# Optimization experiments

Hardware: AMD Instinct MI355X
Metric: run time of the kernel (lower is better)

Reference implementation:

```python
import jax, jax.numpy as jnp
import numpy as np

D_MODEL = 1024
H = 16
D_K = D_MODEL // H
D_FF = 4096
EPS = 1e-5
NEG = -1e9


def setup_inputs() -> dict:
    key = jax.random.key(0)
    ks = jax.random.split(key, 12)
    B, S = 4, 1024
    s = 1.0 / np.sqrt(D_MODEL)
    inp = {
        'x': jax.random.normal(ks[0], (B, S, D_MODEL), dtype=jnp.float32),
        'src_mask': jax.random.randint(ks[1], (B, 1, 1, S), 0, 2, dtype=jnp.int32),
        'wq': jax.random.normal(ks[2], (D_MODEL, D_MODEL), dtype=jnp.float32) * s,
        'bq': jnp.zeros((D_MODEL,), jnp.float32),
        'wk': jax.random.normal(ks[3], (D_MODEL, D_MODEL), dtype=jnp.float32) * s,
        'bk': jnp.zeros((D_MODEL,), jnp.float32),
        'wv': jax.random.normal(ks[4], (D_MODEL, D_MODEL), dtype=jnp.float32) * s,
        'bv': jnp.zeros((D_MODEL,), jnp.float32),
        'wo': jax.random.normal(ks[5], (D_MODEL, D_MODEL), dtype=jnp.float32) * s,
        'bo': jnp.zeros((D_MODEL,), jnp.float32),
        'w1': jax.random.normal(ks[6], (D_MODEL, D_FF), dtype=jnp.float32) * s,
        'b1': jnp.zeros((D_FF,), jnp.float32),
        'w2': jax.random.normal(ks[7], (D_FF, D_MODEL), dtype=jnp.float32) * (1.0 / np.sqrt(D_FF)),
        'b2': jnp.zeros((D_MODEL,), jnp.float32),
        'ln1_a': jnp.ones((1,), jnp.float32),
        'ln1_b': jnp.zeros((1,), jnp.float32),
        'ln2_a': jnp.ones((1,), jnp.float32),
        'ln2_b': jnp.zeros((1,), jnp.float32),
    }
    return inp


def _layernorm(x, alpha, bias):
    # Matches torch: mean over last dim; std is UNBIASED (ddof=1); divide by (std + eps).
    mean = jnp.mean(x, axis=-1, keepdims=True)
    std = jnp.sqrt(jnp.var(x, axis=-1, keepdims=True, ddof=1))
    return alpha * (x - mean) / (std + EPS) + bias


def _attention(xn, src_mask, wq, bq, wk, bk, wv, bv, wo, bo):
    B, S, _ = xn.shape
    q = (xn @ wq + bq).reshape(B, S, H, D_K).transpose(0, 2, 1, 3)  # [B,H,S,Dk]
    k = (xn @ wk + bk).reshape(B, S, H, D_K).transpose(0, 2, 1, 3)
    v = (xn @ wv + bv).reshape(B, S, H, D_K).transpose(0, 2, 1, 3)
    scores = jnp.einsum('bhqd,bhkd->bhqk', q, k) / np.sqrt(D_K)
    scores = jnp.where(src_mask == 0, NEG, scores)
    # NOTE: original module applies NO softmax (faithful to source).
    out = jnp.einsum('bhqk,bhkd->bhqd', scores, v)  # [B,H,S,Dk]
    out = out.transpose(0, 2, 1, 3).reshape(B, S, D_MODEL)
    return out @ wo + bo


def reference(x, src_mask, wq, bq, wk, bk, wv, bv, wo, bo,
              w1, b1, w2, b2, ln1_a, ln1_b, ln2_a, ln2_b):
    # Pre-norm residual 1: self-attention
    x = x + _attention(_layernorm(x, ln1_a, ln1_b), src_mask,
                       wq, bq, wk, bk, wv, bv, wo, bo)
    # Pre-norm residual 2: FFN
    xn = _layernorm(x, ln2_a, ln2_b)
    ffn = jax.nn.relu(xn @ w1 + b1) @ w2 + b2
    return x + ffn
```

## Files before the change

### kernel.cpp

```cpp
#include <hip/hip_runtime.h>
#include <hip/hip_bf16.h>
#include <math.h>


#define EPS 1e-5f

typedef __attribute__((ext_vector_type(8))) short bf16x8;
typedef __attribute__((ext_vector_type(4))) float f32x4;
typedef __attribute__((ext_vector_type(8))) int i32x8;
typedef __attribute__((ext_vector_type(4))) int i32x4;

typedef const __attribute__((address_space(1))) unsigned char glob_byte;
typedef __attribute__((address_space(3))) unsigned char lds_byte;

__device__ __forceinline__ void g2l16(const void* g, void* l) {
  __builtin_amdgcn_global_load_lds((glob_byte*)g, (lds_byte*)l, 16, 0, 0);
}

__device__ __forceinline__ unsigned short f2bf(float f) {
  union { float f; unsigned int u; } v; v.f = f;
  return (unsigned short)((v.u + 0x7FFFu + ((v.u >> 16) & 1u)) >> 16);
}
__device__ __forceinline__ float bf2f(unsigned short b) {
  union { unsigned int u; float f; } v; v.u = (unsigned int)b << 16;
  return v.f;
}
__device__ __forceinline__ unsigned int fbits(float f) {
  union { float f; unsigned int u; } v; v.f = f;
  return v.u;
}
__device__ __forceinline__ unsigned int pk_fp8x4(float a, float b, float c, float d) {
  unsigned int p = 0;
  p = __builtin_amdgcn_cvt_pk_fp8_f32(a, b, p, false);
  p = __builtin_amdgcn_cvt_pk_fp8_f32(c, d, p, true);
  return p;
}

__global__ __launch_bounds__(256) void wconv_ln_kernel(
    const float* __restrict__ wq, const float* __restrict__ wk,
    const float* __restrict__ wv, const float* __restrict__ wo,
    const float* __restrict__ w1, const float* __restrict__ w2,
    const float* __restrict__ bq, const float* __restrict__ bk,
    const float* __restrict__ bv,
    unsigned short* __restrict__ wqkvT, unsigned short* __restrict__ woT,
    unsigned char* __restrict__ w1F8, unsigned char* __restrict__ w2F8,
    float* __restrict__ bqkv,
    const float* __restrict__ x, unsigned short* __restrict__ xn,
    const float* __restrict__ ln1a, const float* __restrict__ ln1b) {
  __shared__ float tile[64][65];
  const int bid = blockIdx.x;
  const int t = threadIdx.x;
  if (bid >= 3073) {
    const int row = bid - 3073;
    const float4 v = ((const float4*)(x + (size_t)row * 1024))[t];
    float s  = v.x + v.y + v.z + v.w;
    float ss = v.x * v.x + v.y * v.y + v.z * v.z + v.w * v.w;
#pragma unroll
    for (int off = 32; off > 0; off >>= 1) {
      s  += __shfl_down(s, off, 64);
      ss += __shfl_down(ss, off, 64);
    }
    __shared__ float red[8];
    const int lane = t & 63, wv_ = t >> 6;
    if (lane == 0) { red[wv_] = s; red[4 + wv_] = ss; }
    __syncthreads();
    const float S  = red[0] + red[1] + red[2] + red[3];
    const float SS = red[4] + red[5] + red[6] + red[7];
    const float mean = S * (1.0f / 1024.0f);
    float var = (SS - 1024.0f * mean * mean) * (1.0f / 1023.0f);
    var = fmaxf(var, 0.0f);
    const float scl = ln1a[0] / (sqrtf(var) + EPS);
    const float b = ln1b[0];
    ushort4 o;
    o.x = f2bf((v.x - mean) * scl + b);
    o.y = f2bf((v.y - mean) * scl + b);
    o.z = f2bf((v.z - mean) * scl + b);
    o.w = f2bf((v.w - mean) * scl + b);
    ((ushort4*)(xn + (size_t)row * 1024))[t] = o;
    return;
  }
  if (bid == 3072) {
#pragma unroll
    for (int i = 0; i < 12; ++i) {
      const int n = i * 256 + t;
      bqkv[n] = n < 1024 ? bq[n] : (n < 2048 ? bk[n - 1024] : bv[n - 2048]);
    }
    return;
  }
  const float* src; int K, N, tk, tn;
  unsigned short* dst16 = nullptr; unsigned char* dst8 = nullptr;
  if (bid < 1024) {
    const int m = bid >> 8, loc = bid & 255;
    src = m == 0 ? wq : m == 1 ? wk : m == 2 ? wv : wo;
    dst16 = m == 3 ? woT : (wqkvT + (size_t)m * 1024 * 1024);
    K = 1024; N = 1024; tk = loc >> 4; tn = loc & 15;
  } else if (bid < 2048) {
    const int loc = bid - 1024; src = w1; dst8 = w1F8;
    K = 1024; N = 4096; tk = loc >> 6; tn = loc & 63;
  } else {
    const int loc = bid - 2048; src = w2; dst8 = w2F8;
    K = 4096; N = 1024; tk = loc >> 4; tn = loc & 15;
  }
  const int lr = t >> 4, lc = (t & 15) * 4;
#pragma unroll
  for (int i = 0; i < 4; ++i) {
    const float4 v = *(const float4*)(src + (size_t)(tk * 64 + lr + 16 * i) * N + tn * 64 + lc);
    tile[lr + 16 * i][lc + 0] = v.x;
    tile[lr + 16 * i][lc + 1] = v.y;
    tile[lr + 16 * i][lc + 2] = v.z;
    tile[lr + 16 * i][lc + 3] = v.w;
  }
  __syncthreads();
  const int on = t >> 2, ok = (t & 3) * 16;
#pragma unroll
  for (int jj = 0; jj < 4; ++jj) {
    if (dst8) {
      const unsigned int p = pk_fp8x4(tile[ok + 4 * jj + 0][on], tile[ok + 4 * jj + 1][on],
                                      tile[ok + 4 * jj + 2][on], tile[ok + 4 * jj + 3][on]);
      *(unsigned int*)(dst8 + (size_t)(tn * 64 + on) * K + tk * 64 + ok + 4 * jj) = p;
    } else {
      ushort4 o4;
      o4.x = f2bf(tile[ok + 4 * jj + 0][on]);
      o4.y = f2bf(tile[ok + 4 * jj + 1][on]);
      o4.z = f2bf(tile[ok + 4 * jj + 2][on]);
      o4.w = f2bf(tile[ok + 4 * jj + 3][on]);
      *(ushort4*)(dst16 + (size_t)(tn * 64 + on) * K + tk * 64 + ok + 4 * jj) = o4;
    }
  }
}

template <int TM, int TN, bool OUT_BF16, bool RELU, bool RES, bool VSPLIT,
          int RX, int RY>
__global__ __launch_bounds__(256, 4) void mfma_gemm(
    const unsigned short* __restrict__ A, const unsigned short* __restrict__ Bt,
    const float* __restrict__ bias, const float* __restrict__ res,
    void* __restrict__ C0, void* __restrict__ C1,
    int N, int lda, int ldb, int KH) {
  constexpr int WM = 2, WN = 2;
  constexpr int MSPAN = TM / WM, NSPAN = TN / WN;
  constexpr int MI = MSPAN / 16, NJ = NSPAN / 16;
  __shared__ __align__(16) unsigned short As[TM * 64];
  __shared__ __align__(16) unsigned short Bs[TN * 64];
  const int tid = threadIdx.x, lane = tid & 63;
  const int w = tid >> 6;
  const int quad = lane >> 4, col = lane & 15;
  const int wm = w % WM, wn = w / WM;

  int bx = blockIdx.x, by = blockIdx.y;
  {
    const int gx = gridDim.x;
    const int L = bx + gx * by;
    const int r = L & 7, s = L >> 3;
    const int nrx = gx / RX;
    const int rx = r % nrx, ry = r / nrx;
    bx = rx * RX + s % RX;
    by = ry * RY + (s / RX) % RY;
  }
  const int m0 = by * TM, n0 = bx * TN;

  f32x4 acc[MI][NJ];
  const f32x4 z4 = {0.f, 0.f, 0.f, 0.f};
#pragma unroll
  for (int i = 0; i < MI; ++i)
#pragma unroll
    for (int j = 0; j < NJ; ++j) acc[i][j] = z4;

  for (int k0 = 0; k0 < KH; k0 += 64) {
    __syncthreads();
#pragma unroll
    for (int t = 0; t < TM / 32; ++t) {
      const int s = t * 256 + tid;
      const int r = s >> 3, c = (s & 7) ^ (r & 7);
      g2l16(A + (size_t)(m0 + r) * lda + k0 + c * 8, (void*)(As + s * 8));
    }
#pragma unroll
    for (int t = 0; t < TN / 32; ++t) {
      const int s = t * 256 + tid;
      const int r = s >> 3, c = (s & 7) ^ (r & 7);
      g2l16(Bt + (size_t)(n0 + r) * ldb + k0 + c * 8, (void*)(Bs + s * 8));
    }
    __syncthreads();
#pragma unroll
    for (int h = 0; h < 2; ++h) {
      bf16x8 af[MI], bfr[NJ];
#pragma unroll
      for (int i = 0; i < MI; ++i) {
        const int rr = wm * MSPAN + i * 16 + col;
        af[i] = *(const bf16x8*)(As + rr * 64 + (((h << 2) | quad) ^ (rr & 7)) * 8);
      }
#pragma unroll
      for (int j = 0; j < NJ; ++j) {
        const int rr = wn * NSPAN + j * 16 + col;
        bfr[j] = *(const bf16x8*)(Bs + rr * 64 + (((h << 2) | quad) ^ (rr & 7)) * 8);
      }
#pragma unroll
      for (int i = 0; i < MI; ++i)
#pragma unroll
        for (int j = 0; j < NJ; ++j)
          acc[i][j] = __builtin_amdgcn_mfma_f32_16x16x32_bf16(af[i], bfr[j], acc[i][j], 0, 0, 0);
    }
  }
#pragma unroll
  for (int i = 0; i < MI; ++i) {
    const int mrow = m0 + wm * MSPAN + i * 16 + quad * 4;
#pragma unroll
    for (int j = 0; j < NJ; ++j) {
      const int n = n0 + wn * NSPAN + j * 16 + col;
      const float bn = bias[n];
      if (VSPLIT && n0 >= 2048) {
        ushort4 o4;
        o4.x = f2bf(acc[i][j][0] + bn);
        o4.y = f2bf(acc[i][j][1] + bn);
        o4.z = f2bf(acc[i][j][2] + bn);
        o4.w = f2bf(acc[i][j][3] + bn);
        *(ushort4*)((unsigned short*)C1 + (size_t)(n - 2048) * 4096 + mrow) = o4;
        continue;
      }
#pragma unroll
      for (int r = 0; r < 4; ++r) {
        const int m = mrow + r;
        float v = acc[i][j][r] + bn;
        if (RES)  v += res[(size_t)m * N + n];
        if (RELU) v = fmaxf(v, 0.f);
        if (OUT_BF16) ((unsigned short*)C0)[(size_t)m * N + n] = f2bf(v);
        else          ((float*)C0)[(size_t)m * N + n] = v;
      }
    }
  }
}

template <bool FP8OUT, int TN, int RX, int RY>
__global__ __launch_bounds__(256, 4) void mfma_gemm_fp8(
    const unsigned char* __restrict__ A, const unsigned char* __restrict__ Bt,
    const float* __restrict__ bias, const unsigned short* __restrict__ res16,
    void* __restrict__ C0, int N, int lda, int ldb, int KH) {
  constexpr int NSPAN = TN / 2;
  constexpr int NJ = NSPAN / 16;
  __shared__ __align__(16) unsigned char As[128 * 128];
  __shared__ __align__(16) unsigned char Bs[TN * 128];
  const int tid = threadIdx.x, lane = tid & 63;
  const int w = tid >> 6;
  const int quad = lane >> 4, col = lane & 15;
  const int wm = w & 1, wn = w >> 1;

  int bx = blockIdx.x, by = blockIdx.y;
  {
    const int gx = gridDim.x;
    const int L = bx + gx * by;
    const int r = L & 7, s = L >> 3;
    const int nrx = gx / RX;
    const int rx = r % nrx, ry = r / nrx;
    bx = rx * RX + s % RX;
    by = ry * RY + (s / RX) % RY;
  }
  const int m0 = by * 128, n0 = bx * TN;

  f32x4 acc[4][NJ];
  const f32x4 z4 = {0.f, 0.f, 0.f, 0.f};
#pragma unroll
  for (int i = 0; i < 4; ++i)
#pragma unroll
    for (int j = 0; j < NJ; ++j) acc[i][j] = z4;

  for (int k0 = 0; k0 < KH; k0 += 128) {
    __syncthreads();
#pragma unroll
    for (int t = 0; t < 4; ++t) {
      const int s = t * 256 + tid;
      const int r = s >> 3, c = (s & 7) ^ (r & 7);
      g2l16(A + (size_t)(m0 + r) * lda + k0 + c * 16, (void*)(As + s * 16));
    }
#pragma unroll
    for (int t = 0; t < TN / 32; ++t) {
      const int s = t * 256 + tid;
      const int r = s >> 3, c = (s & 7) ^ (r & 7);
      g2l16(Bt + (size_t)(n0 + r) * ldb + k0 + c * 16, (void*)(Bs + s * 16));
    }
    __syncthreads();
    i32x8 af[4];
#pragma unroll
    for (int i = 0; i < 4; ++i) {
      const int rr = wm * 64 + i * 16 + col;
      const i32x4* rowp = (const i32x4*)(As + rr * 128);
      const i32x4 lo = rowp[(2 * quad) ^ (rr & 7)];
      const i32x4 hi = rowp[(2 * quad + 1) ^ (rr & 7)];
      af[i] = __builtin_shufflevector(lo, hi, 0, 1, 2, 3, 4, 5, 6, 7);
    }
#pragma unroll
    for (int j = 0; j < NJ; ++j) {
      const int rr = wn * NSPAN + j * 16 + col;
      const i32x4* rowp = (const i32x4*)(Bs + rr * 128);
      const i32x4 lo = rowp[(2 * quad) ^ (rr & 7)];
      const i32x4 hi = rowp[(2 * quad + 1) ^ (rr & 7)];
      const i32x8 bfj = __builtin_shufflevector(lo, hi, 0, 1, 2, 3, 4, 5, 6, 7);
#pragma unroll
      for (int i = 0; i < 4; ++i)
        acc[i][j] = __builtin_amdgcn_mfma_scale_f32_16x16x128_f8f6f4(
            af[i], bfj, acc[i][j], 0, 0, 0, 0x7F7F7F7Fu, 0, 0x7F7F7F7Fu);
    }
  }
#pragma unroll
  for (int i = 0; i < 4; ++i) {
    const int mrow = m0 + wm * 64 + i * 16 + quad * 4;
#pragma unroll
    for (int j = 0; j < NJ; ++j) {
      const int n = n0 + wn * NSPAN + j * 16 + col;
      const float bn = bias[n];
#pragma unroll
      for (int r = 0; r < 4; ++r) {
        const int m = mrow + r;
        if (FP8OUT) {
          const float v = fmaxf(acc[i][j][r] + bn, 0.f);
          const unsigned int p = __builtin_amdgcn_cvt_pk_fp8_f32(v, v, 0, false);
          ((unsigned char*)C0)[(size_t)m * N + n] = (unsigned char)(p & 0xFF);
        } else {
          const float v = acc[i][j][r] + bn + bf2f(res16[(size_t)m * N + n]);
          ((float*)C0)[(size_t)m * N + n] = v;
        }
      }
    }
  }
}

__global__ __launch_bounds__(256) void ln2_kernel(
    const unsigned short* __restrict__ x1,
    const float* __restrict__ alpha, const float* __restrict__ beta,
    unsigned char* __restrict__ xn2f8) {
  const int row = blockIdx.x, t = threadIdx.x;
  const size_t i = (size_t)row * 256 + t;
  const ushort4 a4 = ((const ushort4*)x1)[i];
  float4 v;
  v.x = bf2f(a4.x); v.y = bf2f(a4.y); v.z = bf2f(a4.z); v.w = bf2f(a4.w);
  float s  = v.x + v.y + v.z + v.w;
  float ss = v.x * v.x + v.y * v.y + v.z * v.z + v.w * v.w;
#pragma unroll
  for (int off = 32; off > 0; off >>= 1) {
    s  += __shfl_down(s, off, 64);
    ss += __shfl_down(ss, off, 64);
  }
  __shared__ float red[8];
  const int lane = t & 63, wv_ = t >> 6;
  if (lane == 0) { red[wv_] = s; red[4 + wv_] = ss; }
  __syncthreads();
  const float S  = red[0] + red[1] + red[2] + red[3];
  const float SS = red[4] + red[5] + red[6] + red[7];
  const float mean = S * (1.0f / 1024.0f);
  float var = (SS - 1024.0f * mean * mean) * (1.0f / 1023.0f);
  var = fmaxf(var, 0.0f);
  const float scl = alpha[0] / (sqrtf(var) + EPS);
  const float bb = beta[0];
  ((unsigned int*)xn2f8)[i] = pk_fp8x4((v.x - mean) * scl + bb,
                                       (v.y - mean) * scl + bb,
                                       (v.z - mean) * scl + bb,
                                       (v.w - mean) * scl + bb);
}

__global__ __launch_bounds__(256) void attn_combine_kernel(
    const unsigned short* __restrict__ p0, const unsigned short* __restrict__ p1,
    const float* __restrict__ corr, unsigned short* __restrict__ ctx) {
  const int row = blockIdx.x, t = threadIdx.x;
  const size_t i = (size_t)row * 256 + t;
  const ushort4 a4 = ((const ushort4*)p0)[i];
  const ushort4 b4 = ((const ushort4*)p1)[i];
  const float4 c4 = ((const float4*)(corr + (row >> 10) * 1024))[t];
  ushort4 o;
  o.x = f2bf(bf2f(a4.x) + bf2f(b4.x) - 1e9f * c4.x);
  o.y = f2bf(bf2f(a4.y) + bf2f(b4.y) - 1e9f * c4.y);
  o.z = f2bf(bf2f(a4.z) + bf2f(b4.z) - 1e9f * c4.z);
  o.w = f2bf(bf2f(a4.w) + bf2f(b4.w) - 1e9f * c4.w);
  ((ushort4*)ctx)[i] = o;
}

__global__ __launch_bounds__(256, 4) void attn_masksum_kernel(
    const unsigned short* __restrict__ qkb, const unsigned short* __restrict__ vT,
    const int* __restrict__ mask,
    unsigned short* __restrict__ ctxp0, unsigned short* __restrict__ ctxp1,
    float* __restrict__ corr) {
  __shared__ __align__(16) unsigned short Qs[128 * 64];
  __shared__ __align__(16) unsigned short Ks[32 * 64];
  __shared__ __align__(16) unsigned short Vs[64 * 32];
  __shared__ __align__(16) unsigned short Ps[128 * 40];
  __shared__ float redm[4][4];
  const int tid = threadIdx.x, lane = tid & 63, w = tid >> 6;

  if (blockIdx.z >= 8) {
    const int hd = blockIdx.x + 8 * (blockIdx.y + 16 * (blockIdx.z - 8));
    const int t = tid;
    float sb[4];
#pragma unroll
    for (int b = 0; b < 4; ++b) {
      const ushort4 v4 = *(const ushort4*)(vT + (size_t)hd * 4096 + b * 1024 + t * 4);
      const int4 m4 = *(const int4*)(mask + b * 1024 + t * 4);
      float s = 0.f;
      if (m4.x == 0) s += bf2f(v4.x);
      if (m4.y == 0) s += bf2f(v4.y);
      if (m4.z == 0) s += bf2f(v4.z);
      if (m4.w == 0) s += bf2f(v4.w);
#pragma unroll
      for (int off = 32; off > 0; off >>= 1) s += __shfl_down(s, off, 64);
      sb[b] = s;
    }
    if (lane == 0) {
      redm[w][0] = sb[0]; redm[w][1] = sb[1]; redm[w][2] = sb[2]; redm[w][3] = sb[3];
    }
    __syncthreads();
    if (t < 4)
      corr[t * 1024 + hd] = redm[0][t] + redm[1][t] + redm[2][t] + redm[3][t];
    return;
  }

  const int quad = lane >> 4, col = lane & 15;
  const int L = blockIdx.x + 8 * (blockIdx.y + 16 * blockIdx.z);
  const int s_ = L >> 3;
  const int g = (L & 7) * 16 + (s_ >> 3);
  const int q0 = (s_ & 7) * 128;
  const int h = g & 15, bkz = g >> 4;
  const int b = bkz >> 1, kz = bkz & 1;
  const size_t qbase = ((size_t)(b * 1024 + q0)) * 2048 + h * 64;

#pragma unroll
  for (int t = 0; t < 4; ++t) {
    const int s = t * 256 + w * 64 + lane;
    const int m = s >> 3, c = (s & 7) ^ (m & 7);
    g2l16(qkb + qbase + (size_t)m * 2048 + c * 8, (void*)(Qs + s * 8));
  }
  __syncthreads();
  bf16x8 qf[2][2];
#pragma unroll
  for (int qt = 0; qt < 2; ++qt)
#pragma unroll
    for (int kf = 0; kf < 2; ++kf) {
      const int m = (w * 2 + qt) * 16 + col;
      const int c = (kf * 4 + quad) ^ (m & 7);
      qf[qt][kf] = *(const bf16x8*)(Qs + m * 64 + c * 8);
    }

  const f32x4 z4 = {0.f, 0.f, 0.f, 0.f};
  f32x4 oacc[2][4];
#pragma unroll
  for (int qt = 0; qt < 2; ++qt)
#pragma unroll
    for (int nt = 0; nt < 4; ++nt) oacc[qt][nt] = z4;

  const int* mrow = mask + b * 1024;
  const int kb0 = kz * 512;
  for (int kb = kb0; kb < kb0 + 512; kb += 32) {
    __syncthreads();
    {
      const int s = w * 64 + lane;
      const int key = s >> 3, ck = (s & 7) ^ (key & 7);
      g2l16(qkb + ((size_t)(b * 1024 + kb + key)) * 2048 + 1024 + h * 64 + ck * 8,
            (void*)(Ks + s * 8));
      const int d = s >> 2, cv = (s & 3) ^ (((d >> 2) ^ d) & 3);
      g2l16(vT + ((size_t)(h * 64 + d)) * 4096 + b * 1024 + kb + cv * 8,
            (void*)(Vs + s * 8));
    }
    __syncthreads();

    f32x4 st[2][2];
#pragma unroll
    for (int qt = 0; qt < 2; ++qt)
#pragma unroll
      for (int kt = 0; kt < 2; ++kt) st[qt][kt] = z4;
#pragma unroll
    for (int kt = 0; kt < 2; ++kt)
#pragma unroll
      for (int kf = 0; kf < 2; ++kf) {
        const int key = kt * 16 + col;
        const int c = (kf * 4 + quad) ^ (key & 7);
        const bf16x8 kfrag = *(const bf16x8*)(Ks + key * 64 + c * 8);
#pragma unroll
        for (int qt = 0; qt < 2; ++qt)
          st[qt][kt] = __builtin_amdgcn_mfma_f32_16x16x32_bf16(
              kfrag, qf[qt][kf], st[qt][kt], 0, 0, 0);
      }

    const int4 mv0 = *(const int4*)(mrow + kb + quad * 4);
    const int4 mv1 = *(const int4*)(mrow + kb + 16 + quad * 4);
#pragma unroll
    for (int qt = 0; qt < 2; ++qt) {
      const int qrow = (w * 2 + qt) * 16 + col;
#pragma unroll
      for (int kt = 0; kt < 2; ++kt) {
        const int4 mv = kt ? mv1 : mv0;
        const f32x4 sv = st[qt][kt];
        const unsigned int u0 = fbits((mv.x ? 0.125f : 0.f) * sv[0]) + 0x8000u;
        const unsigned int u1 = fbits((mv.y ? 0.125f : 0.f) * sv[1]) + 0x8000u;
        const unsigned int u2 = fbits((mv.z ? 0.125f : 0.f) * sv[2]) + 0x8000u;
        const unsigned int u3 = fbits((mv.w ? 0.125f : 0.f) * sv[3]) + 0x8000u;
        uint2 pk;
        pk.x = (u0 >> 16) | (u1 & 0xFFFF0000u);
        pk.y = (u2 >> 16) | (u3 & 0xFFFF0000u);
        const int pp = kt * 2 + (quad >> 1);
        *(uint2*)(Ps + qrow * 40 + ((pp ^ (qrow & 3)) * 8 + (quad & 1) * 4)) = pk;
      }
    }

#pragma unroll
    for (int qt = 0; qt < 2; ++qt) {
      const int qrow = (w * 2 + qt) * 16 + col;
      const bf16x8 pf = *(const bf16x8*)(Ps + qrow * 40 + (quad ^ (qrow & 3)) * 8);
#pragma unroll
      for (int nt = 0; nt < 4; ++nt) {
        const int vr = nt * 16 + col;
        const bf16x8 vf = *(const bf16x8*)(Vs + vr * 32 + ((quad ^ (((vr >> 2) ^ vr) & 3))) * 8);
        oacc[qt][nt] = __builtin_amdgcn_mfma_f32_16x16x32_bf16(pf, vf, oacc[qt][nt], 0, 0, 0);
      }
    }
  }

  unsigned short* P = kz ? ctxp1 : ctxp0;
#pragma unroll
  for (int qt = 0; qt < 2; ++qt)
#pragma unroll
    for (int nt = 0; nt < 4; ++nt) {
      const int d = nt * 16 + col;
#pragma unroll
      for (int r = 0; r < 4; ++r) {
        const int qq = q0 + (w * 2 + qt) * 16 + quad * 4 + r;
        P[((size_t)(b * 1024) + qq) * 1024 + h * 64 + d] = f2bf(oacc[qt][nt][r]);
      }
    }
}

extern "C" void kernel_launch(void* const* d_in, const int* in_sizes, int n_in,
                              void* d_out, int out_size, void* d_ws, size_t ws_size,
                              hipStream_t stream) {
  const float* x    = (const float*)d_in[0];
  const int*   mask = (const int*)d_in[1];
  const float* wq = (const float*)d_in[2];
  const float* bq = (const float*)d_in[3];
  const float* wk = (const float*)d_in[4];
  const float* bk = (const float*)d_in[5];
  const float* wv = (const float*)d_in[6];
  const float* bv = (const float*)d_in[7];
  const float* wo = (const float*)d_in[8];
  const float* bo = (const float*)d_in[9];
  const float* w1 = (const float*)d_in[10];
  const float* b1 = (const float*)d_in[11];
  const float* w2 = (const float*)d_in[12];
  const float* b2 = (const float*)d_in[13];
  const float* ln1a = (const float*)d_in[14];
  const float* ln1b = (const float*)d_in[15];
  const float* ln2a = (const float*)d_in[16];
  const float* ln2b = (const float*)d_in[17];
  float* out = (float*)d_out;
  char* W = (char*)d_ws;
  const size_t MB = 1u << 20;

  unsigned short* wqkvT = (unsigned short*)(W + 0 * MB);
  unsigned short* woT   = (unsigned short*)(W + 6 * MB);
  unsigned char*  w1F8  = (unsigned char*)(W + 8 * MB);
  unsigned char*  w2F8  = (unsigned char*)(W + 16 * MB);
  float*          bqkv  = (float*)(W + 24 * MB);
  float*          corr  = (float*)(W + 24 * MB + 65536);
  unsigned short* xn    = (unsigned short*)(W + 25 * MB);
  unsigned char*  xn2f8 = (unsigned char*)(W + 25 * MB);
  unsigned short* qkb   = (unsigned short*)(W + 33 * MB);
  unsigned short* vT    = (unsigned short*)(W + 49 * MB);
  unsigned short* ctxp0 = (unsigned short*)(W + 57 * MB);
  unsigned short* ctxp1 = (unsigned short*)(W + 65 * MB);
  unsigned short* ctx   = (unsigned short*)(W + 33 * MB);
  unsigned short* x1    = (unsigned short*)(W + 73 * MB);
  unsigned char*  hbF8  = (unsigned char*)(W + 49 * MB);

  wconv_ln_kernel<<<7169, 256, 0, stream>>>(wq, wk, wv, wo, w1, w2, bq, bk, bv,
                                            wqkvT, woT, w1F8, w2F8, bqkv,
                                            x, xn, ln1a, ln1b);
  mfma_gemm<128, 128, true, false, false, true, 12, 8>
      <<<dim3(24, 32), 256, 0, stream>>>(
      xn, wqkvT, bqkv, nullptr, qkb, vT, 2048, 1024, 1024, 1024);
  attn_masksum_kernel<<<dim3(8, 16, 16), 256, 0, stream>>>(
      qkb, vT, mask, ctxp0, ctxp1, corr);
  attn_combine_kernel<<<4096, 256, 0, stream>>>(ctxp0, ctxp1, corr, ctx);
  mfma_gemm<128, 64, true, false, true, false, 8, 8>
      <<<dim3(16, 32), 256, 0, stream>>>(
      ctx, woT, bo, x, x1, nullptr, 1024, 1024, 1024, 1024);
  ln2_kernel<<<4096, 256, 0, stream>>>(x1, ln2a, ln2b, xn2f8);
  mfma_gemm_fp8<true, 128, 16, 8><<<dim3(32, 32), 256, 0, stream>>>(
      xn2f8, w1F8, b1, nullptr, hbF8, 4096, 1024, 1024, 1024);
  mfma_gemm_fp8<false, 64, 8, 8><<<dim3(16, 32), 256, 0, stream>>>(
      hbF8, w2F8, b2, x1, out, 1024, 4096, 4096, 4096);
}
```

Before: 280.3 us.

## Reassociate softmax-free attention as Q·(KᵀMV)·Wo with per-batch folded weights

Because the attention has no softmax, scores@V is linear, so the code computes per-(batch,head) 64x64 moments KᵀdiagMask·V once. It folds them into a per-batch projected weight W' = M·Wo, with the masked -1e9 correction folded into a per-batch bias. The output projection GEMM then consumes Q directly with the batched weight, removing the S×S attention kernel and the combine pass. The cost is two small low-parallelism kernels (64 blocks each), extra bf16 rounding of the moments and folded weights, and a per-batch 2 MB weight buffer.

```diff
diff --git a/kernel.cpp b/kernel.cpp
--- a/kernel.cpp
+++ b/kernel.cpp
@@ -24,10 +24,6 @@
 __device__ __forceinline__ float bf2f(unsigned short b) {
   union { unsigned int u; float f; } v; v.u = (unsigned int)b << 16;
   return v.f;
-}
-__device__ __forceinline__ unsigned int fbits(float f) {
-  union { float f; unsigned int u; } v; v.f = f;
-  return v.u;
 }
 __device__ __forceinline__ unsigned int pk_fp8x4(float a, float b, float c, float d) {
   unsigned int p = 0;
@@ -129,8 +125,8 @@
   }
 }
 
-template <int TM, int TN, bool OUT_BF16, bool RELU, bool RES, bool VSPLIT,
-          int RX, int RY>
+template <int TM, int TN, bool OUT_BF16, bool RELU, bool RES, int VSN0,
+          bool BATCHB, int RX, int RY>
 __global__ __launch_bounds__(256, 4) void mfma_gemm(
     const unsigned short* __restrict__ A, const unsigned short* __restrict__ Bt,
     const float* __restrict__ bias, const float* __restrict__ res,
@@ -157,6 +153,11 @@
     by = ry * RY + (s / RX) % RY;
   }
   const int m0 = by * TM, n0 = bx * TN;
+  if (BATCHB) {
+    const int bb = m0 >> 10;
+    Bt += (size_t)bb * 1024 * ldb;
+    bias += bb * 1024;
+  }
 
   f32x4 acc[MI][NJ];
   const f32x4 z4 = {0.f, 0.f, 0.f, 0.f};
@@ -207,13 +208,13 @@
     for (int j = 0; j < NJ; ++j) {
       const int n = n0 + wn * NSPAN + j * 16 + col;
       const float bn = bias[n];
-      if (VSPLIT && n0 >= 2048) {
+      if (VSN0 != 0 && n0 >= VSN0) {
         ushort4 o4;
         o4.x = f2bf(acc[i][j][0] + bn);
         o4.y = f2bf(acc[i][j][1] + bn);
         o4.z = f2bf(acc[i][j][2] + bn);
         o4.w = f2bf(acc[i][j][3] + bn);
-        *(ushort4*)((unsigned short*)C1 + (size_t)(n - 2048) * 4096 + mrow) = o4;
+        *(ushort4*)((unsigned short*)C1 + (size_t)(n - VSN0) * 4096 + mrow) = o4;
         continue;
       }
 #pragma unroll
@@ -355,172 +356,108 @@
                                        (v.w - mean) * scl + bb);
 }
 
-__global__ __launch_bounds__(256) void attn_combine_kernel(
-    const unsigned short* __restrict__ p0, const unsigned short* __restrict__ p1,
-    const float* __restrict__ corr, unsigned short* __restrict__ ctx) {
-  const int row = blockIdx.x, t = threadIdx.x;
-  const size_t i = (size_t)row * 256 + t;
-  const ushort4 a4 = ((const ushort4*)p0)[i];
-  const ushort4 b4 = ((const ushort4*)p1)[i];
-  const float4 c4 = ((const float4*)(corr + (row >> 10) * 1024))[t];
-  ushort4 o;
-  o.x = f2bf(bf2f(a4.x) + bf2f(b4.x) - 1e9f * c4.x);
-  o.y = f2bf(bf2f(a4.y) + bf2f(b4.y) - 1e9f * c4.y);
-  o.z = f2bf(bf2f(a4.z) + bf2f(b4.z) - 1e9f * c4.z);
-  o.w = f2bf(bf2f(a4.w) + bf2f(b4.w) - 1e9f * c4.w);
-  ((ushort4*)ctx)[i] = o;
-}
-
-__global__ __launch_bounds__(256, 4) void attn_masksum_kernel(
-    const unsigned short* __restrict__ qkb, const unsigned short* __restrict__ vT,
-    const int* __restrict__ mask,
-    unsigned short* __restrict__ ctxp0, unsigned short* __restrict__ ctxp1,
-    float* __restrict__ corr) {
-  __shared__ __align__(16) unsigned short Qs[128 * 64];
-  __shared__ __align__(16) unsigned short Ks[32 * 64];
-  __shared__ __align__(16) unsigned short Vs[64 * 32];
-  __shared__ __align__(16) unsigned short Ps[128 * 40];
-  __shared__ float redm[4][4];
+__global__ __launch_bounds__(256) void kv_moment_kernel(
+    const unsigned short* __restrict__ kvT, const int* __restrict__ mask,
+    unsigned short* __restrict__ Mb, float* __restrict__ corr) {
   const int tid = threadIdx.x, lane = tid & 63, w = tid >> 6;
-
-  if (blockIdx.z >= 8) {
-    const int hd = blockIdx.x + 8 * (blockIdx.y + 16 * (blockIdx.z - 8));
-    const int t = tid;
-    float sb[4];
-#pragma unroll
-    for (int b = 0; b < 4; ++b) {
-      const ushort4 v4 = *(const ushort4*)(vT + (size_t)hd * 4096 + b * 1024 + t * 4);
-      const int4 m4 = *(const int4*)(mask + b * 1024 + t * 4);
-      float s = 0.f;
-      if (m4.x == 0) s += bf2f(v4.x);
-      if (m4.y == 0) s += bf2f(v4.y);
-      if (m4.z == 0) s += bf2f(v4.z);
-      if (m4.w == 0) s += bf2f(v4.w);
-#pragma unroll
-      for (int off = 32; off > 0; off >>= 1) s += __shfl_down(s, off, 64);
-      sb[b] = s;
-    }
-    if (lane == 0) {
-      redm[w][0] = sb[0]; redm[w][1] = sb[1]; redm[w][2] = sb[2]; redm[w][3] = sb[3];
-    }
-    __syncthreads();
-    if (t < 4)
-      corr[t * 1024 + hd] = redm[0][t] + redm[1][t] + redm[2][t] + redm[3][t];
-    return;
-  }
-
   const int quad = lane >> 4, col = lane & 15;
-  const int L = blockIdx.x + 8 * (blockIdx.y + 16 * blockIdx.z);
-  const int s_ = L >> 3;
-  const int g = (L & 7) * 16 + (s_ >> 3);
-  const int q0 = (s_ & 7) * 128;
-  const int h = g & 15, bkz = g >> 4;
-  const int b = bkz >> 1, kz = bkz & 1;
-  const size_t qbase = ((size_t)(b * 1024 + q0)) * 2048 + h * 64;
-
-#pragma unroll
-  for (int t = 0; t < 4; ++t) {
-    const int s = t * 256 + w * 64 + lane;
-    const int m = s >> 3, c = (s & 7) ^ (m & 7);
-    g2l16(qkb + qbase + (size_t)m * 2048 + c * 8, (void*)(Qs + s * 8));
-  }
+  const int bh = blockIdx.x, b = bh >> 4, h = bh & 15;
+  const unsigned short* kT  = kvT + (size_t)(h * 64 + w * 16 + col) * 4096 + b * 1024;
+  const unsigned short* vTb = kvT + (size_t)(1024 + h * 64) * 4096 + b * 1024;
+  const int* mrow = mask + b * 1024;
+  const f32x4 z4 = {0.f, 0.f, 0.f, 0.f};
+  f32x4 acc[4] = {z4, z4, z4, z4};
+  float cf[4] = {0.f, 0.f, 0.f, 0.f};
+#pragma unroll 2
+  for (int t0 = 0; t0 < 1024; t0 += 32) {
+    const int tok = t0 + quad * 8;
+    const int4 ma = *(const int4*)(mrow + tok);
+    const int4 mb2 = *(const int4*)(mrow + tok + 4);
+    bf16x8 af = *(const bf16x8*)(kT + tok);
+    af[0] = ma.x  ? af[0] : (short)0;
+    af[1] = ma.y  ? af[1] : (short)0;
+    af[2] = ma.z  ? af[2] : (short)0;
+    af[3] = ma.w  ? af[3] : (short)0;
+    af[4] = mb2.x ? af[4] : (short)0;
+    af[5] = mb2.y ? af[5] : (short)0;
+    af[6] = mb2.z ? af[6] : (short)0;
+    af[7] = mb2.w ? af[7] : (short)0;
+#pragma unroll
+    for (int c = 0; c < 4; ++c) {
+      const bf16x8 vf = *(const bf16x8*)(vTb + (size_t)(c * 16 + col) * 4096 + tok);
+      if (w == 0) {
+        if (!ma.x)  cf[c] += bf2f((unsigned short)vf[0]);
+        if (!ma.y)  cf[c] += bf2f((unsigned short)vf[1]);
+        if (!ma.z)  cf[c] += bf2f((unsigned short)vf[2]);
+        if (!ma.w)  cf[c] += bf2f((unsigned short)vf[3]);
+        if (!mb2.x) cf[c] += bf2f((unsigned short)vf[4]);
+        if (!mb2.y) cf[c] += bf2f((unsigned short)vf[5]);
+        if (!mb2.z) cf[c] += bf2f((unsigned short)vf[6]);
+        if (!mb2.w) cf[c] += bf2f((unsigned short)vf[7]);
+      }
+      acc[c] = __builtin_amdgcn_mfma_f32_16x16x32_bf16(af, vf, acc[c], 0, 0, 0);
+    }
+  }
+  unsigned short* Mrow = Mb + (size_t)bh * 4096;
+#pragma unroll
+  for (int c = 0; c < 4; ++c) {
+#pragma unroll
+    for (int r = 0; r < 4; ++r)
+      Mrow[(w * 16 + quad * 4 + r) * 64 + c * 16 + col] = f2bf(0.125f * acc[c][r]);
+  }
+  if (w == 0) {
+#pragma unroll
+    for (int c = 0; c < 4; ++c) {
+      float s = cf[c];
+      s += __shfl_xor(s, 16, 64);
+      s += __shfl_xor(s, 32, 64);
+      if (quad == 0) corr[b * 1024 + h * 64 + c * 16 + col] = s;
+    }
+  }
+}
+
+__global__ __launch_bounds__(256) void wprime_kernel(
+    const unsigned short* __restrict__ Mb, const unsigned short* __restrict__ woT,
+    const float* __restrict__ corr, const float* __restrict__ bo,
+    unsigned short* __restrict__ Wbt, float* __restrict__ cboW) {
+  __shared__ __align__(16) float corrS[1024];
+  const int tid = threadIdx.x, lane = tid & 63, w = tid >> 6;
+  const int quad = lane >> 4, col = lane & 15;
+  const int blk = blockIdx.x, b = blk >> 4, nt = blk & 15;
+  ((f32x4*)corrS)[tid] = ((const f32x4*)(corr + b * 1024))[tid >> 6 ? tid : tid];
   __syncthreads();
-  bf16x8 qf[2][2];
-#pragma unroll
-  for (int qt = 0; qt < 2; ++qt)
-#pragma unroll
-    for (int kf = 0; kf < 2; ++kf) {
-      const int m = (w * 2 + qt) * 16 + col;
-      const int c = (kf * 4 + quad) ^ (m & 7);
-      qf[qt][kf] = *(const bf16x8*)(Qs + m * 64 + c * 8);
-    }
-
+  const int nbase = nt * 64 + w * 16;
   const f32x4 z4 = {0.f, 0.f, 0.f, 0.f};
-  f32x4 oacc[2][4];
-#pragma unroll
-  for (int qt = 0; qt < 2; ++qt)
-#pragma unroll
-    for (int nt = 0; nt < 4; ++nt) oacc[qt][nt] = z4;
-
-  const int* mrow = mask + b * 1024;
-  const int kb0 = kz * 512;
-  for (int kb = kb0; kb < kb0 + 512; kb += 32) {
-    __syncthreads();
-    {
-      const int s = w * 64 + lane;
-      const int key = s >> 3, ck = (s & 7) ^ (key & 7);
-      g2l16(qkb + ((size_t)(b * 1024 + kb + key)) * 2048 + 1024 + h * 64 + ck * 8,
-            (void*)(Ks + s * 8));
-      const int d = s >> 2, cv = (s & 3) ^ (((d >> 2) ^ d) & 3);
-      g2l16(vT + ((size_t)(h * 64 + d)) * 4096 + b * 1024 + kb + cv * 8,
-            (void*)(Vs + s * 8));
-    }
-    __syncthreads();
-
-    f32x4 st[2][2];
-#pragma unroll
-    for (int qt = 0; qt < 2; ++qt)
-#pragma unroll
-      for (int kt = 0; kt < 2; ++kt) st[qt][kt] = z4;
-#pragma unroll
-    for (int kt = 0; kt < 2; ++kt)
-#pragma unroll
-      for (int kf = 0; kf < 2; ++kf) {
-        const int key = kt * 16 + col;
-        const int c = (kf * 4 + quad) ^ (key & 7);
-        const bf16x8 kfrag = *(const bf16x8*)(Ks + key * 64 + c * 8);
-#pragma unroll
-        for (int qt = 0; qt < 2; ++qt)
-          st[qt][kt] = __builtin_amdgcn_mfma_f32_16x16x32_bf16(
-              kfrag, qf[qt][kf], st[qt][kt], 0, 0, 0);
-      }
-
-    const int4 mv0 = *(const int4*)(mrow + kb + quad * 4);
-    const int4 mv1 = *(const int4*)(mrow + kb + 16 + quad * 4);
-#pragma unroll
-    for (int qt = 0; qt < 2; ++qt) {
-      const int qrow = (w * 2 + qt) * 16 + col;
-#pragma unroll
-      for (int kt = 0; kt < 2; ++kt) {
-        const int4 mv = kt ? mv1 : mv0;
-        const f32x4 sv = st[qt][kt];
-        const unsigned int u0 = fbits((mv.x ? 0.125f : 0.f) * sv[0]) + 0x8000u;
-        const unsigned int u1 = fbits((mv.y ? 0.125f : 0.f) * sv[1]) + 0x8000u;
-        const unsigned int u2 = fbits((mv.z ? 0.125f : 0.f) * sv[2]) + 0x8000u;
-        const unsigned int u3 = fbits((mv.w ? 0.125f : 0.f) * sv[3]) + 0x8000u;
-        uint2 pk;
-        pk.x = (u0 >> 16) | (u1 & 0xFFFF0000u);
-        pk.y = (u2 >> 16) | (u3 & 0xFFFF0000u);
-        const int pp = kt * 2 + (quad >> 1);
-        *(uint2*)(Ps + qrow * 40 + ((pp ^ (qrow & 3)) * 8 + (quad & 1) * 4)) = pk;
-      }
-    }
-
-#pragma unroll
-    for (int qt = 0; qt < 2; ++qt) {
-      const int qrow = (w * 2 + qt) * 16 + col;
-      const bf16x8 pf = *(const bf16x8*)(Ps + qrow * 40 + (quad ^ (qrow & 3)) * 8);
-#pragma unroll
-      for (int nt = 0; nt < 4; ++nt) {
-        const int vr = nt * 16 + col;
-        const bf16x8 vf = *(const bf16x8*)(Vs + vr * 32 + ((quad ^ (((vr >> 2) ^ vr) & 3))) * 8);
-        oacc[qt][nt] = __builtin_amdgcn_mfma_f32_16x16x32_bf16(pf, vf, oacc[qt][nt], 0, 0, 0);
-      }
-    }
-  }
-
-  unsigned short* P = kz ? ctxp1 : ctxp0;
-#pragma unroll
-  for (int qt = 0; qt < 2; ++qt)
-#pragma unroll
-    for (int nt = 0; nt < 4; ++nt) {
-      const int d = nt * 16 + col;
-#pragma unroll
-      for (int r = 0; r < 4; ++r) {
-        const int qq = q0 + (w * 2 + qt) * 16 + quad * 4 + r;
-        P[((size_t)(b * 1024) + qq) * 1024 + h * 64 + d] = f2bf(oacc[qt][nt][r]);
-      }
-    }
+  unsigned short* Wb = Wbt + (size_t)b * 1048576;
+#pragma unroll 1
+  for (int h = 0; h < 16; ++h) {
+    const bf16x8 af0 = *(const bf16x8*)(woT + (size_t)(nbase + col) * 1024 + h * 64 + quad * 8);
+    const bf16x8 af1 = *(const bf16x8*)(woT + (size_t)(nbase + col) * 1024 + h * 64 + 32 + quad * 8);
+    const unsigned short* Mrow = Mb + (size_t)(b * 16 + h) * 4096;
+#pragma unroll
+    for (int dt = 0; dt < 4; ++dt) {
+      const bf16x8 bf0 = *(const bf16x8*)(Mrow + (dt * 16 + col) * 64 + quad * 8);
+      const bf16x8 bf1 = *(const bf16x8*)(Mrow + (dt * 16 + col) * 64 + 32 + quad * 8);
+      f32x4 a = __builtin_amdgcn_mfma_f32_16x16x32_bf16(af0, bf0, z4, 0, 0, 0);
+      a = __builtin_amdgcn_mfma_f32_16x16x32_bf16(af1, bf1, a, 0, 0, 0);
+#pragma unroll
+      for (int r = 0; r < 4; ++r)
+        Wb[(size_t)(nbase + quad * 4 + r) * 1024 + h * 64 + dt * 16 + col] = f2bf(a[r]);
+    }
+  }
+  const int rr = tid >> 2, q = tid & 3;
+  const int n = nt * 64 + rr;
+  float s = 0.f;
+  const unsigned short* wrow = woT + (size_t)n * 1024;
+#pragma unroll 4
+  for (int k = q * 256; k < q * 256 + 256; k += 4) {
+    const ushort4 w4 = *(const ushort4*)(wrow + k);
+    s += bf2f(w4.x) * corrS[k] + bf2f(w4.y) * corrS[k + 1] +
+         bf2f(w4.z) * corrS[k + 2] + bf2f(w4.w) * corrS[k + 3];
+  }
+  s += __shfl_xor(s, 1, 64);
+  s += __shfl_xor(s, 2, 64);
+  if (q == 0) cboW[b * 1024 + n] = bo[n] - 1e9f * s;
 }
 
 extern "C" void kernel_launch(void* const* d_in, const int* in_sizes, int n_in,
@@ -554,28 +491,27 @@
   unsigned char*  w2F8  = (unsigned char*)(W + 16 * MB);
   float*          bqkv  = (float*)(W + 24 * MB);
   float*          corr  = (float*)(W + 24 * MB + 65536);
+  float*          cboW  = (float*)(W + 24 * MB + 131072);
+  unsigned short* Mb    = (unsigned short*)(W + 24 * MB + 262144);
   unsigned short* xn    = (unsigned short*)(W + 25 * MB);
   unsigned char*  xn2f8 = (unsigned char*)(W + 25 * MB);
-  unsigned short* qkb   = (unsigned short*)(W + 33 * MB);
-  unsigned short* vT    = (unsigned short*)(W + 49 * MB);
-  unsigned short* ctxp0 = (unsigned short*)(W + 57 * MB);
-  unsigned short* ctxp1 = (unsigned short*)(W + 65 * MB);
-  unsigned short* ctx   = (unsigned short*)(W + 33 * MB);
-  unsigned short* x1    = (unsigned short*)(W + 73 * MB);
-  unsigned char*  hbF8  = (unsigned char*)(W + 49 * MB);
+  unsigned short* qRM   = (unsigned short*)(W + 33 * MB);
+  unsigned short* kvT   = (unsigned short*)(W + 41 * MB);
+  unsigned short* Wbt   = (unsigned short*)(W + 57 * MB);
+  unsigned short* x1    = (unsigned short*)(W + 65 * MB);
+  unsigned char*  hbF8  = (unsigned char*)(W + 41 * MB);
 
   wconv_ln_kernel<<<7169, 256, 0, stream>>>(wq, wk, wv, wo, w1, w2, bq, bk, bv,
                                             wqkvT, woT, w1F8, w2F8, bqkv,
                                             x, xn, ln1a, ln1b);
-  mfma_gemm<128, 128, true, false, false, true, 12, 8>
+  mfma_gemm<128, 128, true, false, false, 1024, false, 12, 8>
       <<<dim3(24, 32), 256, 0, stream>>>(
-      xn, wqkvT, bqkv, nullptr, qkb, vT, 2048, 1024, 1024, 1024);
-  attn_masksum_kernel<<<dim3(8, 16, 16), 256, 0, stream>>>(
-      qkb, vT, mask, ctxp0, ctxp1, corr);
-  attn_combine_kernel<<<4096, 256, 0, stream>>>(ctxp0, ctxp1, corr, ctx);
-  mfma_gemm<128, 64, true, false, true, false, 8, 8>
+      xn, wqkvT, bqkv, nullptr, qRM, kvT, 1024, 1024, 1024, 1024);
+  kv_moment_kernel<<<64, 256, 0, stream>>>(kvT, mask, Mb, corr);
+  wprime_kernel<<<64, 256, 0, stream>>>(Mb, woT, corr, bo, Wbt, cboW);
+  mfma_gemm<128, 64, true, false, true, 0, true, 8, 8>
       <<<dim3(16, 32), 256, 0, stream>>>(
-      ctx, woT, bo, x, x1, nullptr, 1024, 1024, 1024, 1024);
+      qRM, Wbt, cboW, x, x1, nullptr, 1024, 1024, 1024, 1024);
   ln2_kernel<<<4096, 256, 0, stream>>>(x1, ln2a, ln2b, xn2f8);
   mfma_gemm_fp8<true, 128, 16, 8><<<dim3(32, 32), 256, 0, stream>>>(
       xn2f8, w1F8, b1, nullptr, hbF8, 4096, 1024, 1024, 1024);
```

Result: slower. 307.8 us (+9.8%).
